# Performance work log

Measured on AMD Instinct MI355X. Metric: run time of the kernel, lower is better.

Reference implementation:

```python
import jax, jax.numpy as jnp
import numpy as np

D = 768
H = 8
HD = D // H  # 96
DFF = 2048
EPS = 1e-5


def layernorm(x, g, b):
    mu = jnp.mean(x, axis=-1, keepdims=True)
    var = jnp.var(x, axis=-1, keepdims=True)
    return (x - mu) * jax.lax.rsqrt(var + EPS) * g + b


def setup_inputs() -> dict:
    key = jax.random.key(0)
    ks = jax.random.split(key, 12)
    B, L = 4, 1024
    s = lambda fan: 1.0 / np.sqrt(fan)
    return {
        "x": jax.random.normal(ks[0], (B, L, D), jnp.float32),
        "attn_bias": jax.random.normal(ks[1], (B, L, L), jnp.float32),
        "in_proj_w": jax.random.normal(ks[2], (3 * D, D), jnp.float32) * s(D),
        "in_proj_b": jnp.zeros((3 * D,), jnp.float32),
        "out_w": jax.random.normal(ks[3], (D, D), jnp.float32) * s(D),
        "out_b": jnp.zeros((D,), jnp.float32),
        "ff1_w": jax.random.normal(ks[4], (DFF, D), jnp.float32) * s(D),
        "ff1_b": jnp.zeros((DFF,), jnp.float32),
        "ff2_w": jax.random.normal(ks[5], (D, DFF), jnp.float32) * s(DFF),
        "ff2_b": jnp.zeros((D,), jnp.float32),
        "ln1_g": jnp.ones((D,), jnp.float32),
        "ln1_b": jnp.zeros((D,), jnp.float32),
        "ln2_g": jnp.ones((D,), jnp.float32),
        "ln2_b": jnp.zeros((D,), jnp.float32),
    }


def reference(x, attn_bias, in_proj_w, in_proj_b, out_w, out_b,
              ff1_w, ff1_b, ff2_w, ff2_b, ln1_g, ln1_b, ln2_g, ln2_b):
    B, L, _ = x.shape
    # combined QKV projection (torch nn.MultiheadAttention in_proj)
    qkv = x @ in_proj_w.T + in_proj_b  # [B,L,3D]
    q, k, v = jnp.split(qkv, 3, axis=-1)
    q = q.reshape(B, L, H, HD).transpose(0, 2, 1, 3)  # [B,H,L,hd]
    k = k.reshape(B, L, H, HD).transpose(0, 2, 1, 3)
    v = v.reshape(B, L, H, HD).transpose(0, 2, 1, 3)
    scale = 1.0 / np.sqrt(HD)
    scores = jnp.einsum('bhld,bhmd->bhlm', q, k) * scale + attn_bias[:, None, :, :]
    probs = jax.nn.softmax(scores, axis=-1)
    attn = jnp.einsum('bhlm,bhmd->bhld', probs, v)  # [B,H,L,hd]
    attn = attn.transpose(0, 2, 1, 3).reshape(B, L, D)
    attn = attn @ out_w.T + out_b
    x = layernorm(x + attn, ln1_g, ln1_b)
    h = jax.nn.gelu(x @ ff1_w.T + ff1_b, approximate=False) @ ff2_w.T + ff2_b
    x = layernorm(x + h, ln2_g, ln2_b)
    return x
```

## Files before the change

kernel.cpp:

```cpp
#include <hip/hip_runtime.h>

typedef __bf16 bf16x8 __attribute__((ext_vector_type(8)));
typedef float f32x4 __attribute__((ext_vector_type(4)));
typedef unsigned short u16x8 __attribute__((ext_vector_type(8)));
typedef short s16x4 __attribute__((ext_vector_type(4)));

__device__ __forceinline__ unsigned short f2b(float f) {
    union { float f; unsigned u; } v; v.f = f;
    unsigned r = (v.u + 0x7fffu + ((v.u >> 16) & 1u)) >> 16;
    return (unsigned short)r;
}

__device__ __forceinline__ float b2f(unsigned short b) {
    union { unsigned u; float f; } v; v.u = ((unsigned)b) << 16;
    return v.f;
}

__device__ __forceinline__ void load_lds16(const void* g, void* l) {
    __builtin_amdgcn_global_load_lds(
        (const __attribute__((address_space(1))) unsigned int*)g,
        (__attribute__((address_space(3))) unsigned int*)l,
        16, 0, 0);
}

__global__ void cvt5_kernel(const float* __restrict__ s0, const float* __restrict__ s1,
                            const float* __restrict__ s2, const float* __restrict__ s3,
                            const float* __restrict__ s4,
                            unsigned short* __restrict__ d0, unsigned short* __restrict__ d1,
                            unsigned short* __restrict__ d2, unsigned short* __restrict__ d3,
                            unsigned short* __restrict__ d4) {
    int i = blockIdx.x * 256 + threadIdx.x;
    const float* s; unsigned short* d; int off;
    if (i < 786432)       { s = s0; d = d0; off = 0; }
    else if (i < 1228800) { s = s1; d = d1; off = 786432; }
    else if (i < 1376256) { s = s2; d = d2; off = 1228800; }
    else if (i < 1769472) { s = s3; d = d3; off = 1376256; }
    else                  { s = s4; d = d4; off = 1769472; }
    i -= off;
    f32x4 v = ((const f32x4*)s)[i];
    s16x4 o;
    o.x = (short)f2b(v.x);
    o.y = (short)f2b(v.y);
    o.z = (short)f2b(v.z);
    o.w = (short)f2b(v.w);
    ((s16x4*)d)[i] = o;
}

__global__ void expb_kernel(const float* __restrict__ bias, unsigned short* __restrict__ eb, int n4) {
    int i = blockIdx.x * 256 + threadIdx.x;
    if (i < n4) {
        f32x4 v = ((const f32x4*)bias)[i];
        s16x4 o;
#pragma unroll
        for (int e = 0; e < 4; e++) o[e] = (short)f2b(__expf(v[e]));
        ((s16x4*)eb)[i] = o;
    }
}

template <int EPI>
__global__ __launch_bounds__(256, 5)
void gemm_ho(const unsigned short* __restrict__ A, const unsigned short* __restrict__ Bm,
             const float* __restrict__ bias, void* __restrict__ Cout,
             int M, int N, int K) {
    __shared__ unsigned short As[2][64 * 64];
    __shared__ unsigned short Bs[2][64 * 64];
    const int tid = threadIdx.x, lane = tid & 63, wid = tid >> 6;
    const int l15 = lane & 15, lq = lane >> 4;
    const int wr = wid >> 1, wc = wid & 1;

    const int nwg = gridDim.x * gridDim.y;
    int bid = blockIdx.y * gridDim.x + blockIdx.x;
    bid = (bid & 7) * (nwg >> 3) + (bid >> 3);
    const int bx = bid % gridDim.x, by = bid / gridDim.x;
    const int m0 = by * 64, n0 = bx * 64;

    const int srow = lane >> 3;
    const int scol = ((lane & 7) ^ srow) * 8;
    const int sw = (l15 & 7) << 4;

    f32x4 acc[2][2];
#pragma unroll
    for (int i = 0; i < 2; i++)
#pragma unroll
        for (int j = 0; j < 2; j++) acc[i][j] = 0.0f;

    auto stage = [&](int buf, int kt) {
        const int kb = kt * 64;
#pragma unroll
        for (int i = 0; i < 4; ++i) {
            const int c = wid * 4 + i;
            if (c < 8) {
                load_lds16(A + (size_t)(m0 + c * 8 + srow) * K + kb + scol,
                           (char*)As[buf] + c * 1024);
            } else {
                load_lds16(Bm + (size_t)(n0 + (c - 8) * 8 + srow) * K + kb + scol,
                           (char*)Bs[buf] + (c - 8) * 1024);
            }
        }
    };

    auto compute = [&](int buf) {
#pragma unroll
        for (int kc = 0; kc < 2; ++kc) {
            const int cb = kc * 64;
            bf16x8 af[2], bf[2];
#pragma unroll
            for (int mi = 0; mi < 2; mi++) {
                const int row = wr * 32 + mi * 16 + l15;
                af[mi] = *(const bf16x8*)((const char*)As[buf] + row * 128 + ((cb + lq * 16) ^ sw));
            }
#pragma unroll
            for (int ni = 0; ni < 2; ni++) {
                const int row = wc * 32 + ni * 16 + l15;
                bf[ni] = *(const bf16x8*)((const char*)Bs[buf] + row * 128 + ((cb + lq * 16) ^ sw));
            }
#pragma unroll
            for (int mi = 0; mi < 2; mi++)
#pragma unroll
                for (int ni = 0; ni < 2; ni++)
                    acc[mi][ni] = __builtin_amdgcn_mfma_f32_16x16x32_bf16(af[mi], bf[ni], acc[mi][ni], 0, 0, 0);
        }
    };

    const int nkt = K / 64;
    stage(0, 0);
    stage(1, 1);
    asm volatile("s_waitcnt vmcnt(4)" ::: "memory");
    __builtin_amdgcn_s_barrier();
    int cur = 0;
    for (int t = 0; t < nkt; ++t) {
        compute(cur);
        __builtin_amdgcn_s_barrier();
        if (t + 2 < nkt) {
            stage(cur, t + 2);
            asm volatile("s_waitcnt vmcnt(4)" ::: "memory");
        } else if (t + 1 < nkt) {
            asm volatile("s_waitcnt vmcnt(0)" ::: "memory");
        }
        if (t + 1 < nkt) __builtin_amdgcn_s_barrier();
        cur ^= 1;
    }

#pragma unroll
    for (int mi = 0; mi < 2; mi++) {
#pragma unroll
        for (int ni = 0; ni < 2; ni++) {
            const int col = n0 + wc * 32 + ni * 16 + l15;
            const float bv = bias[col];
#pragma unroll
            for (int r = 0; r < 4; r++) {
                const int row = m0 + wr * 32 + mi * 16 + lq * 4 + r;
                float v = acc[mi][ni][r] + bv;
                if constexpr (EPI == 2) {
                    v = 0.5f * v * (1.0f + erff(v * 0.7071067811865475f));
                }
                if constexpr (EPI == 1) {
                    ((float*)Cout)[(size_t)row * N + col] = v;
                } else {
                    ((unsigned short*)Cout)[(size_t)row * N + col] = f2b(v);
                }
            }
        }
    }
}

__global__ __launch_bounds__(256, 2)
void attn_kernel(const unsigned short* __restrict__ qkv,
                 const unsigned short* __restrict__ eb,
                 unsigned short* __restrict__ out) {
    const int L = 1024, TD = 2304, HD = 96;
    const int qt = blockIdx.x, h = blockIdx.y, b = blockIdx.z;
    const int tid = threadIdx.x, lane = tid & 63, wid = tid >> 6;
    const int l15 = lane & 15, lq = lane >> 4;
    const int q0 = qt * 64;
    const float scale = 0.10206207261596576f;

    __shared__ char smem[45568];
    unsigned short (*Ks)[104]    = (unsigned short (*)[104])smem;
    unsigned short (*Vt)[72]     = (unsigned short (*)[72])(smem + 13312);
    unsigned short (*Ps)[16][72] = (unsigned short (*)[16][72])(smem + 27136);
    unsigned short (*Ebs)[72]    = (unsigned short (*)[72])(smem + 36352);
    float (*Ot)[16][100]         = (float (*)[16][100])smem;

    bf16x8 qf[3];
    const int qrow = q0 + wid * 16 + l15;
#pragma unroll
    for (int kc = 0; kc < 3; kc++)
        qf[kc] = *(const bf16x8*)(qkv + (size_t)(b * L + qrow) * TD + h * HD + kc * 32 + lq * 8);

    int krow[3], kcc[3];
#pragma unroll
    for (int i = 0; i < 3; i++) { int c = i * 256 + tid; krow[i] = c / 12; kcc[i] = c % 12; }
    int erow[2], ech[2];
#pragma unroll
    for (int i = 0; i < 2; i++) { int c = i * 256 + tid; erow[i] = c >> 3; ech[i] = c & 7; }

    f32x4 kreg[3]; u16x8 vreg[3]; u16x8 ereg[2];
    auto issue = [&](int kv0) {
#pragma unroll
        for (int i = 0; i < 3; i++)
            kreg[i] = *(const f32x4*)(qkv + (size_t)(b * L + kv0 + krow[i]) * TD + 768 + h * HD + kcc[i] * 8);
#pragma unroll
        for (int i = 0; i < 3; i++)
            vreg[i] = *(const u16x8*)(qkv + (size_t)(b * L + kv0 + lane) * TD + 1536 + h * HD + (i * 4 + wid) * 8);
#pragma unroll
        for (int i = 0; i < 2; i++)
            ereg[i] = *(const u16x8*)(eb + (size_t)(b * L + q0 + erow[i]) * L + kv0 + ech[i] * 8);
    };
    auto commit = [&]() {
#pragma unroll
        for (int i = 0; i < 3; i++) *(f32x4*)&Ks[krow[i]][kcc[i] * 8] = kreg[i];
#pragma unroll
        for (int i = 0; i < 3; i++) {
            const int dblk = i * 4 + wid;
#pragma unroll
            for (int j = 0; j < 8; j++) Vt[dblk * 8 + j][lane] = vreg[i][j];
        }
#pragma unroll
        for (int i = 0; i < 2; i++) *(u16x8*)&Ebs[erow[i]][ech[i] * 8] = ereg[i];
    };

    f32x4 o[6];
#pragma unroll
    for (int df = 0; df < 6; df++) o[df] = 0.0f;
    float lsum[4] = {0.f, 0.f, 0.f, 0.f};

    issue(0);
    for (int t = 0; t < 16; ++t) {
        asm volatile("s_waitcnt vmcnt(0)" ::: "memory");
        commit();
        asm volatile("s_waitcnt lgkmcnt(0)" ::: "memory");
        __builtin_amdgcn_s_barrier();

        f32x4 s[4];
#pragma unroll
        for (int nf = 0; nf < 4; nf++) s[nf] = 0.0f;
#pragma unroll
        for (int kc = 0; kc < 3; kc++) {
#pragma unroll
            for (int nf = 0; nf < 4; nf++) {
                bf16x8 kf = *(const bf16x8*)&Ks[nf * 16 + l15][kc * 32 + lq * 8];
                s[nf] = __builtin_amdgcn_mfma_f32_16x16x32_bf16(qf[kc], kf, s[nf], 0, 0, 0);
            }
        }
        if (t + 1 < 16) issue((t + 1) * 64);

#pragma unroll
        for (int nf = 0; nf < 4; nf++) {
#pragma unroll
            for (int r = 0; r < 4; r++) {
                float ebv = b2f(Ebs[wid * 16 + lq * 4 + r][nf * 16 + l15]);
                float p = __expf(s[nf][r] * scale) * ebv;
                s[nf][r] = p;
                lsum[r] += p;
            }
        }
#pragma unroll
        for (int nf = 0; nf < 4; nf++)
#pragma unroll
            for (int r = 0; r < 4; r++)
                Ps[wid][lq * 4 + r][nf * 16 + l15] = f2b(s[nf][r]);
        asm volatile("s_waitcnt lgkmcnt(0)" ::: "memory");
#pragma unroll
        for (int kc = 0; kc < 2; kc++) {
            bf16x8 pf = *(const bf16x8*)&Ps[wid][l15][kc * 32 + lq * 8];
#pragma unroll
            for (int df = 0; df < 6; df++) {
                bf16x8 vf = *(const bf16x8*)&Vt[df * 16 + l15][kc * 32 + lq * 8];
                o[df] = __builtin_amdgcn_mfma_f32_16x16x32_bf16(pf, vf, o[df], 0, 0, 0);
            }
        }
        __builtin_amdgcn_s_barrier();
    }

#pragma unroll
    for (int r = 0; r < 4; r++) {
#pragma unroll
        for (int d = 1; d < 16; d <<= 1) lsum[r] += __shfl_xor(lsum[r], d, 64);
    }

#pragma unroll
    for (int r = 0; r < 4; r++) {
        float inv = 1.0f / lsum[r];
        const int rl = lq * 4 + r;
#pragma unroll
        for (int df = 0; df < 6; df++) {
            const int cl = df * 16 + l15;
            Ot[wid][rl][cl ^ (lq << 3)] = o[df][r] * inv;
        }
    }
    asm volatile("s_waitcnt lgkmcnt(0)" ::: "memory");
    {
        const int r = lane >> 2, c8 = lane & 3;
        const int rowg = q0 + wid * 16 + r;
#pragma unroll
        for (int it = 0; it < 3; it++) {
            const int oc = c8 + 4 * it;
            const int po = oc ^ ((r >> 2) & 3);
            f32x4 a = *(const f32x4*)&Ot[wid][r][po * 8];
            f32x4 bb = *(const f32x4*)&Ot[wid][r][po * 8 + 4];
            u16x8 p;
#pragma unroll
            for (int e = 0; e < 4; e++) { p[e] = f2b(a[e]); p[e + 4] = f2b(bb[e]); }
            *(u16x8*)&out[((size_t)b * L + rowg) * 768 + h * 96 + oc * 8] = p;
        }
    }
}

template <int WRITE_B>
__global__ __launch_bounds__(256, 4)
void ln_kernel(const float* __restrict__ x, const float* __restrict__ res,
               const float* __restrict__ g, const float* __restrict__ bvec,
               float* __restrict__ outf, unsigned short* __restrict__ outb) {
    const int Dm = 768;
    int row = blockIdx.x;
    int tid = threadIdx.x;
    f32x4 v = {0.f, 0.f, 0.f, 0.f};
    float sum = 0.f, sq = 0.f;
    if (tid < 192) {
        f32x4 xv = ((const f32x4*)(x + (size_t)row * Dm))[tid];
        f32x4 rv = ((const f32x4*)(res + (size_t)row * Dm))[tid];
        v = xv + rv;
        sum = v.x + v.y + v.z + v.w;
        sq = v.x * v.x + v.y * v.y + v.z * v.z + v.w * v.w;
    }
#pragma unroll
    for (int d = 1; d < 64; d <<= 1) {
        sum += __shfl_xor(sum, d, 64);
        sq += __shfl_xor(sq, d, 64);
    }
    __shared__ float ps[8];
    int lane = tid & 63, wid = tid >> 6;
    if (lane == 0) { ps[wid] = sum; ps[wid + 4] = sq; }
    __syncthreads();
    sum = ps[0] + ps[1] + ps[2] + ps[3];
    sq = ps[4] + ps[5] + ps[6] + ps[7];
    float mu = sum * (1.0f / 768.0f);
    float var = sq * (1.0f / 768.0f) - mu * mu;
    float rsg = rsqrtf(var + 1e-5f);
    if (tid < 192) {
        f32x4 gv = ((const f32x4*)g)[tid];
        f32x4 bv = ((const f32x4*)bvec)[tid];
        f32x4 ov;
#pragma unroll
        for (int e = 0; e < 4; e++) ov[e] = (v[e] - mu) * rsg * gv[e] + bv[e];
        ((f32x4*)(outf + (size_t)row * Dm))[tid] = ov;
        if constexpr (WRITE_B) {
            s16x4 pb;
#pragma unroll
            for (int e = 0; e < 4; e++) pb[e] = (short)f2b(ov[e]);
            ((s16x4*)(outb + (size_t)row * Dm))[tid] = pb;
        }
    }
}

extern "C" void kernel_launch(void* const* d_in, const int* in_sizes, int n_in,
                              void* d_out, int out_size, void* d_ws, size_t ws_size,
                              hipStream_t stream) {
    (void)in_sizes; (void)n_in; (void)out_size; (void)ws_size;
    const float* x         = (const float*)d_in[0];
    const float* attn_bias = (const float*)d_in[1];
    const float* in_proj_w = (const float*)d_in[2];
    const float* in_proj_b = (const float*)d_in[3];
    const float* out_w     = (const float*)d_in[4];
    const float* out_b     = (const float*)d_in[5];
    const float* ff1_w     = (const float*)d_in[6];
    const float* ff1_b     = (const float*)d_in[7];
    const float* ff2_w     = (const float*)d_in[8];
    const float* ff2_b     = (const float*)d_in[9];
    const float* ln1_g     = (const float*)d_in[10];
    const float* ln1_b     = (const float*)d_in[11];
    const float* ln2_g     = (const float*)d_in[12];
    const float* ln2_b     = (const float*)d_in[13];

    const int NTOK = 4096;
    char* ws = (char*)d_ws;
    size_t off = 0;
    auto alloc = [&](size_t bytes) { void* p = ws + off; off += (bytes + 255) & ~(size_t)255; return p; };
    unsigned short* xb    = (unsigned short*)alloc((size_t)NTOK * 768 * 2);
    unsigned short* wqkv  = (unsigned short*)alloc((size_t)2304 * 768 * 2);
    unsigned short* wout  = (unsigned short*)alloc((size_t)768 * 768 * 2);
    unsigned short* wff1  = (unsigned short*)alloc((size_t)2048 * 768 * 2);
    unsigned short* wff2  = (unsigned short*)alloc((size_t)768 * 2048 * 2);
    unsigned short* qkvb  = (unsigned short*)alloc((size_t)NTOK * 2304 * 2);
    unsigned short* attnb = (unsigned short*)alloc((size_t)NTOK * 768 * 2);
    float*          aproj = (float*)alloc((size_t)NTOK * 768 * 4);
    float*          x1f   = (float*)alloc((size_t)NTOK * 768 * 4);
    unsigned short* x1b   = (unsigned short*)alloc((size_t)NTOK * 768 * 2);
    unsigned short* h1b  = qkvb;
    float*          ff2o = aproj;
    unsigned short* ebuf = (unsigned short*)aproj;

    cvt5_kernel<<<dim3(8448), 256, 0, stream>>>(x, in_proj_w, out_w, ff1_w, ff2_w,
                                                xb, wqkv, wout, wff1, wff2);
    expb_kernel<<<dim3(4096), 256, 0, stream>>>(attn_bias, ebuf, 1048576);

    gemm_ho<0><<<dim3(2304 / 64, NTOK / 64), 256, 0, stream>>>(xb, wqkv, in_proj_b, qkvb, NTOK, 2304, 768);
    attn_kernel<<<dim3(16, 8, 4), 256, 0, stream>>>(qkvb, ebuf, attnb);
    gemm_ho<1><<<dim3(768 / 64, NTOK / 64), 256, 0, stream>>>(attnb, wout, out_b, aproj, NTOK, 768, 768);
    ln_kernel<1><<<dim3(NTOK), 256, 0, stream>>>(x, aproj, ln1_g, ln1_b, x1f, x1b);
    gemm_ho<2><<<dim3(2048 / 64, NTOK / 64), 256, 0, stream>>>(x1b, wff1, ff1_b, h1b, NTOK, 2048, 768);
    gemm_ho<1><<<dim3(768 / 64, NTOK / 64), 256, 0, stream>>>(h1b, wff2, ff2_b, ff2o, NTOK, 768, 2048);
    ln_kernel<0><<<dim3(NTOK), 256, 0, stream>>>(x1f, ff2o, ln2_g, ln2_b, (float*)d_out, nullptr);
}
```

Before: 165.4 us.

## Double-buffer K/V tiles in LDS and load bias directly into registers

The attention kernel now alternates between two LDS buffers for K and V, which removes the end-of-iteration barrier. The exp(bias) tile is no longer staged through LDS; each lane loads the 16 bias values it needs straight from global memory into registers, one iteration ahead. This drops the bias LDS traffic and one barrier per tile, but LDS use grows to about 62KB and the bias loads become scalar 2-byte gathers, which may hurt coalescing and occupancy.

```diff
diff --git a/kernel.cpp b/kernel.cpp
--- a/kernel.cpp
+++ b/kernel.cpp
@@ -175,11 +175,10 @@
     const int q0 = qt * 64;
     const float scale = 0.10206207261596576f;
 
-    __shared__ char smem[45568];
-    unsigned short (*Ks)[104]    = (unsigned short (*)[104])smem;
-    unsigned short (*Vt)[72]     = (unsigned short (*)[72])(smem + 13312);
-    unsigned short (*Ps)[16][72] = (unsigned short (*)[16][72])(smem + 27136);
-    unsigned short (*Ebs)[72]    = (unsigned short (*)[72])(smem + 36352);
+    __shared__ char smem[63488];
+    auto KsP = [&](int p) { return (unsigned short (*)[104])(smem + p * 13312); };
+    auto VtP = [&](int p) { return (unsigned short (*)[72])(smem + 26624 + p * 13824); };
+    unsigned short (*Ps)[16][72] = (unsigned short (*)[16][72])(smem + 54272);
     float (*Ot)[16][100]         = (float (*)[16][100])smem;
 
     bf16x8 qf[3];
@@ -191,23 +190,29 @@
     int krow[3], kcc[3];
 #pragma unroll
     for (int i = 0; i < 3; i++) { int c = i * 256 + tid; krow[i] = c / 12; kcc[i] = c % 12; }
-    int erow[2], ech[2];
-#pragma unroll
-    for (int i = 0; i < 2; i++) { int c = i * 256 + tid; erow[i] = c >> 3; ech[i] = c & 7; }
-
-    f32x4 kreg[3]; u16x8 vreg[3]; u16x8 ereg[2];
-    auto issue = [&](int kv0) {
+
+    f32x4 kreg[3]; u16x8 vreg[3];
+    unsigned short ereg[4][4];
+    const unsigned short* ebbase = eb + (size_t)(b * L + q0 + wid * 16 + lq * 4) * L;
+
+    auto issueKV = [&](int kv0) {
 #pragma unroll
         for (int i = 0; i < 3; i++)
             kreg[i] = *(const f32x4*)(qkv + (size_t)(b * L + kv0 + krow[i]) * TD + 768 + h * HD + kcc[i] * 8);
 #pragma unroll
         for (int i = 0; i < 3; i++)
             vreg[i] = *(const u16x8*)(qkv + (size_t)(b * L + kv0 + lane) * TD + 1536 + h * HD + (i * 4 + wid) * 8);
-#pragma unroll
-        for (int i = 0; i < 2; i++)
-            ereg[i] = *(const u16x8*)(eb + (size_t)(b * L + q0 + erow[i]) * L + kv0 + ech[i] * 8);
     };
-    auto commit = [&]() {
+    auto issueEB = [&](int kv0) {
+#pragma unroll
+        for (int r = 0; r < 4; r++)
+#pragma unroll
+            for (int nf = 0; nf < 4; nf++)
+                ereg[r][nf] = ebbase[(size_t)r * L + kv0 + nf * 16 + l15];
+    };
+    auto commitKV = [&](int p) {
+        unsigned short (*Ks)[104] = KsP(p);
+        unsigned short (*Vt)[72] = VtP(p);
 #pragma unroll
         for (int i = 0; i < 3; i++) *(f32x4*)&Ks[krow[i]][kcc[i] * 8] = kreg[i];
 #pragma unroll
@@ -216,8 +221,6 @@
 #pragma unroll
             for (int j = 0; j < 8; j++) Vt[dblk * 8 + j][lane] = vreg[i][j];
         }
-#pragma unroll
-        for (int i = 0; i < 2; i++) *(u16x8*)&Ebs[erow[i]][ech[i] * 8] = ereg[i];
     };
 
     f32x4 o[6];
@@ -225,13 +228,17 @@
     for (int df = 0; df < 6; df++) o[df] = 0.0f;
     float lsum[4] = {0.f, 0.f, 0.f, 0.f};
 
-    issue(0);
+    issueKV(0);
+    issueEB(0);
     for (int t = 0; t < 16; ++t) {
+        const int p = t & 1;
         asm volatile("s_waitcnt vmcnt(0)" ::: "memory");
-        commit();
+        commitKV(p);
         asm volatile("s_waitcnt lgkmcnt(0)" ::: "memory");
         __builtin_amdgcn_s_barrier();
 
+        unsigned short (*Ks)[104] = KsP(p);
+        unsigned short (*Vt)[72] = VtP(p);
         f32x4 s[4];
 #pragma unroll
         for (int nf = 0; nf < 4; nf++) s[nf] = 0.0f;
@@ -243,18 +250,19 @@
                 s[nf] = __builtin_amdgcn_mfma_f32_16x16x32_bf16(qf[kc], kf, s[nf], 0, 0, 0);
             }
         }
-        if (t + 1 < 16) issue((t + 1) * 64);
+        if (t + 1 < 16) issueKV((t + 1) * 64);
 
 #pragma unroll
         for (int nf = 0; nf < 4; nf++) {
 #pragma unroll
             for (int r = 0; r < 4; r++) {
-                float ebv = b2f(Ebs[wid * 16 + lq * 4 + r][nf * 16 + l15]);
-                float p = __expf(s[nf][r] * scale) * ebv;
-                s[nf][r] = p;
-                lsum[r] += p;
-            }
-        }
+                float p2 = __expf(s[nf][r] * scale) * b2f(ereg[r][nf]);
+                s[nf][r] = p2;
+                lsum[r] += p2;
+            }
+        }
+        if (t + 1 < 16) issueEB((t + 1) * 64);
+
 #pragma unroll
         for (int nf = 0; nf < 4; nf++)
 #pragma unroll
@@ -270,8 +278,8 @@
                 o[df] = __builtin_amdgcn_mfma_f32_16x16x32_bf16(pf, vf, o[df], 0, 0, 0);
             }
         }
-        __builtin_amdgcn_s_barrier();
-    }
+    }
+    __builtin_amdgcn_s_barrier();
 
 #pragma unroll
     for (int r = 0; r < 4; r++) {
```

New measurement: 162.1 us. 2.0% less time.
